# Optimization experiments

Measured on AMD Instinct MI355X. Metric: run time of the kernel, lower is better.

The kernel has to match this reference:

```python
import jax, jax.numpy as jnp
import numpy as np

D_MODEL = 1024
NUM_HEADS = 16
D_K = D_MODEL // NUM_HEADS
THETA = 10000.0


def _rope(x, pos):
    # x: [B, H, S, D_K], pos: [S]
    angles = 1.0 / (THETA ** (jnp.arange(0, D_K, 2, dtype=jnp.float32) / D_K))  # [D_K/2]
    ang = pos.astype(jnp.float32)[:, None] * angles  # [S, D_K/2]
    cos = jnp.repeat(jnp.cos(ang), 2, axis=-1)  # [S, D_K]
    sin = jnp.repeat(jnp.sin(ang), 2, axis=-1)
    x2 = x.reshape(*x.shape[:-1], D_K // 2, 2)
    xr = jnp.stack([-x2[..., 1], x2[..., 0]], axis=-1).reshape(x.shape)
    return x * cos + xr * sin


def setup_inputs() -> dict:
    key = jax.random.key(0)
    ks = jax.random.split(key, 5)
    B, S = 2, 2048
    sd = np.sqrt(2.0 / (D_MODEL + D_MODEL))
    return {
        "x": jax.random.normal(ks[0], (B, S, D_MODEL), dtype=jnp.float32),
        "token_positions": jnp.arange(S, dtype=jnp.int32),
        "Wq": jax.random.normal(ks[1], (D_MODEL, D_MODEL), dtype=jnp.float32) * sd,
        "Wk": jax.random.normal(ks[2], (D_MODEL, D_MODEL), dtype=jnp.float32) * sd,
        "Wv": jax.random.normal(ks[3], (D_MODEL, D_MODEL), dtype=jnp.float32) * sd,
        "Wo": jax.random.normal(ks[4], (D_MODEL, D_MODEL), dtype=jnp.float32) * sd,
    }


def reference(x, token_positions, Wq, Wk, Wv, Wo):
    B, S, _ = x.shape

    def proj_heads(W):
        y = jnp.einsum('bsd,ed->bse', x, W)  # weight stored [d_out, d_in]
        return y.reshape(B, S, NUM_HEADS, D_K).transpose(0, 2, 1, 3)  # [B,H,S,Dk]

    q = _rope(proj_heads(Wq), token_positions)
    k = _rope(proj_heads(Wk), token_positions)
    v = proj_heads(Wv)

    scores = jnp.einsum('bhqd,bhkd->bhqk', q, k) / np.sqrt(D_K)  # [B,H,S,S]
    causal = jnp.tril(jnp.ones((S, S), dtype=bool))
    scores = jnp.where(causal, scores, -jnp.inf)
    attn = jax.nn.softmax(scores, axis=-1)
    out = jnp.einsum('bhqk,bhkd->bhqd', attn, v)  # [B,H,S,Dk]
    out = out.transpose(0, 2, 1, 3).reshape(B, S, D_MODEL)
    return jnp.einsum('bsd,ed->bse', out, Wo)
```

## Files before the change

kernel.cpp:

```cpp
#include <hip/hip_runtime.h>
#include <hip/hip_bf16.h>
#include <cstdint>
#include <cmath>

#define SEQ 2048
#define NH 16
#define DM 1024
#define BATCH 2

typedef short bf16x8 __attribute__((ext_vector_type(8)));
typedef float f32x4 __attribute__((ext_vector_type(4)));
typedef const void __attribute__((address_space(1)))* gas_t;
typedef void __attribute__((address_space(3)))* las_t;

#if __has_builtin(__builtin_amdgcn_exp2f)
#define EXP2(x) __builtin_amdgcn_exp2f(x)
#else
#define EXP2(x) __expf((x) * 0.6931471805599453f)
#endif

#define QSCALE 0.18033688011112042f

static __device__ __forceinline__ unsigned short f2bf(float f) {
    union { __hip_bfloat16 h; unsigned short u; } cv;
    cv.h = __float2bfloat16(f);
    return cv.u;
}
static __device__ __forceinline__ float bf2f(unsigned short u) {
    union { unsigned short u; __hip_bfloat16 h; } cv;
    cv.u = u;
    return __bfloat162float(cv.h);
}

static __device__ __forceinline__ void gload_lds16(const void* g, void* l) {
    __builtin_amdgcn_global_load_lds(
        reinterpret_cast<gas_t>(reinterpret_cast<uintptr_t>(g)),
        reinterpret_cast<las_t>(reinterpret_cast<uintptr_t>(l)),
        16, 0, 0);
}

__global__ __launch_bounds__(256) void cvt_all(
    const float* __restrict__ x,  const float* __restrict__ wq,
    const float* __restrict__ wk, const float* __restrict__ wv,
    const float* __restrict__ wo,
    unsigned short* __restrict__ xb, unsigned short* __restrict__ wqkv,
    unsigned short* __restrict__ wob) {
    int blk = blockIdx.x;
    const float* src; unsigned short* dst; int base;
    if (blk < 4096)      { src = x;  dst = xb;              base = blk; }
    else if (blk < 5120) { src = wq; dst = wqkv;            base = blk - 4096; }
    else if (blk < 6144) { src = wk; dst = wqkv + 1048576;  base = blk - 5120; }
    else if (blk < 7168) { src = wv; dst = wqkv + 2097152;  base = blk - 6144; }
    else                 { src = wo; dst = wob;             base = blk - 7168; }
    int i = base * 256 + threadIdx.x;
    float4 v = reinterpret_cast<const float4*>(src)[i];
    ushort4 o;
    o.x = f2bf(v.x); o.y = f2bf(v.y); o.z = f2bf(v.z); o.w = f2bf(v.w);
    reinterpret_cast<ushort4*>(dst)[i] = o;
}

template<int OUT_BF16>
__global__ __launch_bounds__(256) void gemm_bt(
    const unsigned short* __restrict__ A,
    const unsigned short* __restrict__ B,
    void* __restrict__ C, int M, int N, int K) {
    __shared__ unsigned short As[128 * 32];
    __shared__ unsigned short Bs[128 * 32];
    const int tid = threadIdx.x;
    const int lane = tid & 63, wid = tid >> 6;
    const int wr = wid >> 1, wc = wid & 1;
    const int ln15 = lane & 15, kq = lane >> 4;
    const int bm = blockIdx.y, bn = blockIdx.x;

    f32x4 acc[4][4] = {};
    const int nk = K >> 5;
    for (int kt = 0; kt < nk; ++kt) {
        #pragma unroll
        for (int i = 0; i < 2; ++i) {
            int c = i * 256 + tid;
            int row = c >> 2, k8 = (c & 3) << 3;
            size_t gofsA = (size_t)(bm * 128 + row) * K + kt * 32 + k8;
            size_t gofsB = (size_t)(bn * 128 + row) * K + kt * 32 + k8;
            unsigned ldsoff = (unsigned)(i * 256 + wid * 64) * 16;
            gload_lds16(A + gofsA, (char*)As + ldsoff);
            gload_lds16(B + gofsB, (char*)Bs + ldsoff);
        }
        __syncthreads();
        bf16x8 af[4], bf[4];
        #pragma unroll
        for (int m = 0; m < 4; ++m)
            af[m] = *reinterpret_cast<const bf16x8*>(&As[(wr * 64 + m * 16 + ln15) * 32 + kq * 8]);
        #pragma unroll
        for (int n = 0; n < 4; ++n)
            bf[n] = *reinterpret_cast<const bf16x8*>(&Bs[(wc * 64 + n * 16 + ln15) * 32 + kq * 8]);
        #pragma unroll
        for (int m = 0; m < 4; ++m)
            #pragma unroll
            for (int n = 0; n < 4; ++n)
                acc[m][n] = __builtin_amdgcn_mfma_f32_16x16x32_bf16(af[m], bf[n], acc[m][n], 0, 0, 0);
        __syncthreads();
    }
    #pragma unroll
    for (int m = 0; m < 4; ++m) {
        #pragma unroll
        for (int n = 0; n < 4; ++n) {
            int col = bn * 128 + wc * 64 + n * 16 + ln15;
            #pragma unroll
            for (int j = 0; j < 4; ++j) {
                int row = bm * 128 + wr * 64 + m * 16 + kq * 4 + j;
                if constexpr (OUT_BF16 != 0)
                    ((unsigned short*)C)[(size_t)row * N + col] = f2bf(acc[m][n][j]);
                else
                    ((float*)C)[(size_t)row * N + col] = acc[m][n][j];
            }
        }
    }
}

__global__ __launch_bounds__(256) void rope_table(const int* __restrict__ pos,
                                                  float2* __restrict__ tab) {
    int idx = blockIdx.x * 256 + threadIdx.x;
    int s = idx >> 5, i = idx & 31;
    float fpos = (float)pos[s];
    float freq = exp2f(-(float)i * (13.287712379549449f / 32.0f));
    float ang = fpos * freq, sn, cs;
    sincosf(ang, &sn, &cs);
    tab[idx] = make_float2(cs, sn);
}

__global__ __launch_bounds__(256) void rope_kernel(
    const unsigned short* __restrict__ qkv, const float2* __restrict__ tab,
    unsigned short* __restrict__ Qh, unsigned short* __restrict__ Kh) {
    int bs = blockIdx.x;
    int b = bs >> 11, s = bs & (SEQ - 1);
    int t = threadIdx.x;
    #pragma unroll
    for (int p = t; p < 512; p += 256) {
        int h = p >> 5, i = p & 31;
        float2 cs = tab[(s << 5) + i];
        size_t src = (size_t)bs * 3072 + h * 64 + 2 * i;
        size_t dst = ((size_t)(b * NH + h) * SEQ + s) * 64 + 2 * i;
        ushort2 qv = *reinterpret_cast<const ushort2*>(qkv + src);
        float q0 = bf2f(qv.x), q1 = bf2f(qv.y);
        ushort2 qo;
        qo.x = f2bf((q0 * cs.x - q1 * cs.y) * QSCALE);
        qo.y = f2bf((q1 * cs.x + q0 * cs.y) * QSCALE);
        *reinterpret_cast<ushort2*>(Qh + dst) = qo;
        ushort2 kv = *reinterpret_cast<const ushort2*>(qkv + src + 1024);
        float k0 = bf2f(kv.x), k1 = bf2f(kv.y);
        ushort2 ko;
        ko.x = f2bf(k0 * cs.x - k1 * cs.y);
        ko.y = f2bf(k1 * cs.x + k0 * cs.y);
        *reinterpret_cast<ushort2*>(Kh + dst) = ko;
    }
}

__global__ __launch_bounds__(256) void vtrans_kernel(
    const unsigned short* __restrict__ qkv, unsigned short* __restrict__ Vo) {
    __shared__ unsigned short tile[64][65];
    int blk = blockIdx.x;
    int st = blk & 31, bh = blk >> 5;
    int sb = st * 64;
    int t = threadIdx.x;
    int b = bh >> 4, h = bh & 15;
    #pragma unroll
    for (int u = t; u < 1024; u += 256) {
        int sl = u >> 4, d4 = (u & 15) << 2;
        ushort4 v = *reinterpret_cast<const ushort4*>(
            qkv + (size_t)(b * SEQ + sb + sl) * 3072 + 2048 + h * 64 + d4);
        tile[sl][d4] = v.x; tile[sl][d4 + 1] = v.y;
        tile[sl][d4 + 2] = v.z; tile[sl][d4 + 3] = v.w;
    }
    __syncthreads();
    #pragma unroll
    for (int u = t; u < 1024; u += 256) {
        int d = u >> 4, s4 = (u & 15) << 2;
        ushort4 o;
        o.x = tile[s4][d]; o.y = tile[s4 + 1][d];
        o.z = tile[s4 + 2][d]; o.w = tile[s4 + 3][d];
        *reinterpret_cast<ushort4*>(Vo + ((size_t)bh * 64 + d) * SEQ + sb + s4) = o;
    }
}

__global__ __launch_bounds__(128) void attn_kernel(
    const unsigned short* __restrict__ Qh, const unsigned short* __restrict__ Kh,
    const unsigned short* __restrict__ Vt, unsigned short* __restrict__ Out) {
    __shared__ unsigned short Kb[2][32 * 64];
    __shared__ unsigned short Vb[2][64 * 32];
    __shared__ unsigned short Plds[2][16 * 40];

    const int tid = threadIdx.x;
    const int wid = tid >> 6, lane = tid & 63;
    const int ln15 = lane & 15, g = lane >> 4;
    const int bid = blockIdx.x;
    const int bh = bid & 31;
    const int band = 63 - (bid >> 5);
    const int qb = band * 32 + wid * 16;
    const int nt = band + 1;

    const unsigned short* Qp = Qh + (size_t)bh * SEQ * 64;
    const unsigned short* Kp = Kh + (size_t)bh * SEQ * 64;
    const unsigned short* Vp = Vt + (size_t)bh * 64 * SEQ;
    unsigned short* P = Plds[wid];

    const int c0 = tid, c1 = tid + 128;
    const unsigned short* kSrc0 = Kp + (size_t)(c0 >> 3) * 64 + (((c0 & 7) ^ ((c0 >> 3) & 7)) << 3);
    const unsigned short* kSrc1 = Kp + (size_t)(c1 >> 3) * 64 + (((c1 & 7) ^ ((c1 >> 3) & 7)) << 3);
    const unsigned short* vSrc0 = Vp + (size_t)(c0 >> 2) * SEQ + (((c0 & 3) ^ (((c0 >> 2) >> 1) & 3)) << 3);
    const unsigned short* vSrc1 = Vp + (size_t)(c1 >> 2) * SEQ + (((c1 & 3) ^ (((c1 >> 2) >> 1) & 3)) << 3);
    const unsigned base0 = (unsigned)wid * 1024;
    const unsigned base1 = 2048 + (unsigned)wid * 1024;

    auto stage = [&](int kb, int buf) {
        gload_lds16(kSrc0 + (size_t)kb * 64, (char*)Kb[buf] + base0);
        gload_lds16(kSrc1 + (size_t)kb * 64, (char*)Kb[buf] + base1);
        gload_lds16(vSrc0 + kb, (char*)Vb[buf] + base0);
        gload_lds16(vSrc1 + kb, (char*)Vb[buf] + base1);
    };

    const int r0 = ln15, r1 = ln15 + 16;
    const unsigned kOff0a = r0 * 128 + ((g ^ (r0 & 7)) << 4);
    const unsigned kOff0b = r0 * 128 + (((4 + g) ^ (r0 & 7)) << 4);
    const unsigned kOff1a = r1 * 128 + ((g ^ (r1 & 7)) << 4);
    const unsigned kOff1b = r1 * 128 + (((4 + g) ^ (r1 & 7)) << 4);
    unsigned vOff[4];
    #pragma unroll
    for (int c = 0; c < 4; ++c) {
        int d = c * 16 + ln15;
        vOff[c] = d * 64 + ((g ^ ((d >> 1) & 3)) << 4);
    }

    bf16x8 aq0 = *reinterpret_cast<const bf16x8*>(Qp + (size_t)(qb + ln15) * 64 + g * 8);
    bf16x8 aq1 = *reinterpret_cast<const bf16x8*>(Qp + (size_t)(qb + ln15) * 64 + 32 + g * 8);

    f32x4 oacc[4] = {};
    float lsum = 0.f;
    const int thr = qb + ln15 - 4 * g;

    stage(0, 0);

    for (int t = 0; t < nt; ++t) {
        const int kb = t << 5;
        const int cur = t & 1, nxt = cur ^ 1;
        {
            int tn = t + 1; if (tn > nt - 1) tn = nt - 1;
            stage(tn << 5, nxt);
        }
        asm volatile("s_waitcnt vmcnt(4)" ::: "memory");
        __builtin_amdgcn_s_barrier();

        const unsigned short* K0 = Kb[cur];
        const unsigned short* V0 = Vb[cur];
        const f32x4 z = {};
        bf16x8 kf0 = *reinterpret_cast<const bf16x8*>((const char*)K0 + kOff0a);
        bf16x8 kf1 = *reinterpret_cast<const bf16x8*>((const char*)K0 + kOff0b);
        bf16x8 kf2 = *reinterpret_cast<const bf16x8*>((const char*)K0 + kOff1a);
        bf16x8 kf3 = *reinterpret_cast<const bf16x8*>((const char*)K0 + kOff1b);
        f32x4 s0, s1;
        s0 = __builtin_amdgcn_mfma_f32_16x16x32_bf16(kf0, aq0, z, 0, 0, 0);
        s0 = __builtin_amdgcn_mfma_f32_16x16x32_bf16(kf1, aq1, s0, 0, 0, 0);
        s1 = __builtin_amdgcn_mfma_f32_16x16x32_bf16(kf2, aq0, z, 0, 0, 0);
        s1 = __builtin_amdgcn_mfma_f32_16x16x32_bf16(kf3, aq1, s1, 0, 0, 0);

        float p0[4], p1[4];
        if (t == band) {
            #pragma unroll
            for (int j = 0; j < 4; ++j) {
                p0[j] = (j <= thr - kb) ? EXP2(s0[j]) : 0.f;
                p1[j] = (j <= thr - kb - 16) ? EXP2(s1[j]) : 0.f;
            }
        } else {
            #pragma unroll
            for (int j = 0; j < 4; ++j) { p0[j] = EXP2(s0[j]); p1[j] = EXP2(s1[j]); }
        }
        lsum += (p0[0] + p0[1]) + (p0[2] + p0[3]) + (p1[0] + p1[1]) + (p1[2] + p1[3]);

        ushort4 w0, w1;
        w0.x = f2bf(p0[0]); w0.y = f2bf(p0[1]); w0.z = f2bf(p0[2]); w0.w = f2bf(p0[3]);
        w1.x = f2bf(p1[0]); w1.y = f2bf(p1[1]); w1.z = f2bf(p1[2]); w1.w = f2bf(p1[3]);
        *reinterpret_cast<ushort4*>(&P[ln15 * 40 + 4 * g]) = w0;
        *reinterpret_cast<ushort4*>(&P[ln15 * 40 + 16 + 4 * g]) = w1;
        asm volatile("s_waitcnt lgkmcnt(0)" ::: "memory");
        bf16x8 ap = *reinterpret_cast<const bf16x8*>(&P[ln15 * 40 + 8 * g]);
        #pragma unroll
        for (int c = 0; c < 4; ++c) {
            bf16x8 bv = *reinterpret_cast<const bf16x8*>((const char*)V0 + vOff[c]);
            oacc[c] = __builtin_amdgcn_mfma_f32_16x16x32_bf16(ap, bv, oacc[c], 0, 0, 0);
        }
        asm volatile("s_waitcnt lgkmcnt(0)" ::: "memory");
        __builtin_amdgcn_s_barrier();
    }

    float r = lsum;
    r += __shfl_xor(r, 16);
    r += __shfl_xor(r, 32);
    float linv = 1.f / r;
    float invj[4];
    #pragma unroll
    for (int j = 0; j < 4; ++j)
        invj[j] = __shfl(linv, 20 * g + j);

    int b = bh >> 4, h = bh & 15;
    #pragma unroll
    for (int c = 0; c < 4; ++c)
        #pragma unroll
        for (int j = 0; j < 4; ++j) {
            int s = qb + g * 4 + j;
            Out[((size_t)(b * SEQ + s)) * DM + h * 64 + c * 16 + ln15] =
                f2bf(oacc[c][j] * invj[j]);
        }
}

extern "C" void kernel_launch(void* const* d_in, const int* in_sizes, int n_in,
                              void* d_out, int out_size, void* d_ws, size_t ws_size,
                              hipStream_t stream) {
    const float* x = (const float*)d_in[0];
    const int* pos = (const int*)d_in[1];
    const float* Wq = (const float*)d_in[2];
    const float* Wk = (const float*)d_in[3];
    const float* Wv = (const float*)d_in[4];
    const float* Wo = (const float*)d_in[5];
    float* out = (float*)d_out;

    char* ws = (char*)d_ws;
    const size_t MB = 1024 * 1024;
    unsigned short* xb   = (unsigned short*)(ws + 0 * MB);
    unsigned short* wqkv = (unsigned short*)(ws + 8 * MB);
    unsigned short* wob  = (unsigned short*)(ws + 14 * MB);
    unsigned short* qkv  = (unsigned short*)(ws + 16 * MB);
    float2*         tab  = (float2*)       (ws + 40 * MB);
    unsigned short* qh   = (unsigned short*)(ws + 41 * MB);
    unsigned short* kh   = (unsigned short*)(ws + 49 * MB);
    unsigned short* vtr  = (unsigned short*)(ws + 57 * MB);
    unsigned short* att  = (unsigned short*)(ws + 65 * MB);

    cvt_all<<<8192, 256, 0, stream>>>(x, Wq, Wk, Wv, Wo, xb, wqkv, wob);
    rope_table<<<256, 256, 0, stream>>>(pos, tab);

    gemm_bt<1><<<dim3(24, 32), 256, 0, stream>>>(xb, wqkv, qkv, 4096, 3072, 1024);

    rope_kernel<<<4096, 256, 0, stream>>>(qkv, tab, qh, kh);
    vtrans_kernel<<<1024, 256, 0, stream>>>(qkv, vtr);

    attn_kernel<<<2048, 128, 0, stream>>>(qh, kh, vtr, att);

    gemm_bt<0><<<dim3(8, 32), 256, 0, stream>>>(att, wob, out, 4096, 1024, 1024);
}
```

Baseline: 133.0 us.

## Pair low and high causal query bands per block to balance work and share K/V

Each attention block now handles two query bands, fold and 63-fold, so every block walks the same number of key tiles and the staged K/V tiles are reused by both bands. The grid is halved to 1024 blocks. This balances causal workload across blocks and halves K/V loads for the low band. In exchange each thread holds more registers for two Q fragments and two accumulators, and there are fewer blocks to fill the GPU.

Result: no change. 130.8 us (-1.6%).

```diff
diff --git a/kernel.cpp b/kernel.cpp
--- a/kernel.cpp
+++ b/kernel.cpp
@@ -187,21 +187,23 @@
     const unsigned short* __restrict__ Vt, unsigned short* __restrict__ Out) {
     __shared__ unsigned short Kb[2][32 * 64];
     __shared__ unsigned short Vb[2][64 * 32];
-    __shared__ unsigned short Plds[2][16 * 40];
+    __shared__ unsigned short Plds[2][2][16 * 40];
 
     const int tid = threadIdx.x;
     const int wid = tid >> 6, lane = tid & 63;
     const int ln15 = lane & 15, g = lane >> 4;
     const int bid = blockIdx.x;
     const int bh = bid & 31;
-    const int band = 63 - (bid >> 5);
-    const int qb = band * 32 + wid * 16;
-    const int nt = band + 1;
+    const int fold = bid >> 5;
+    const int qbL = fold * 32 + wid * 16;
+    const int qbH = (63 - fold) * 32 + wid * 16;
+    const int nt = 64 - fold;
 
     const unsigned short* Qp = Qh + (size_t)bh * SEQ * 64;
     const unsigned short* Kp = Kh + (size_t)bh * SEQ * 64;
     const unsigned short* Vp = Vt + (size_t)bh * 64 * SEQ;
-    unsigned short* P = Plds[wid];
+    unsigned short* PL = Plds[wid][0];
+    unsigned short* PH = Plds[wid][1];
 
     const int c0 = tid, c1 = tid + 128;
     const unsigned short* kSrc0 = Kp + (size_t)(c0 >> 3) * 64 + (((c0 & 7) ^ ((c0 >> 3) & 7)) << 3);
@@ -230,12 +232,15 @@
         vOff[c] = d * 64 + ((g ^ ((d >> 1) & 3)) << 4);
     }
 
-    bf16x8 aq0 = *reinterpret_cast<const bf16x8*>(Qp + (size_t)(qb + ln15) * 64 + g * 8);
-    bf16x8 aq1 = *reinterpret_cast<const bf16x8*>(Qp + (size_t)(qb + ln15) * 64 + 32 + g * 8);
-
-    f32x4 oacc[4] = {};
-    float lsum = 0.f;
-    const int thr = qb + ln15 - 4 * g;
+    bf16x8 aqL0 = *reinterpret_cast<const bf16x8*>(Qp + (size_t)(qbL + ln15) * 64 + g * 8);
+    bf16x8 aqL1 = *reinterpret_cast<const bf16x8*>(Qp + (size_t)(qbL + ln15) * 64 + 32 + g * 8);
+    bf16x8 aqH0 = *reinterpret_cast<const bf16x8*>(Qp + (size_t)(qbH + ln15) * 64 + g * 8);
+    bf16x8 aqH1 = *reinterpret_cast<const bf16x8*>(Qp + (size_t)(qbH + ln15) * 64 + 32 + g * 8);
+
+    f32x4 oaccL[4] = {}, oaccH[4] = {};
+    float lsumL = 0.f, lsumH = 0.f;
+    const int thrL = qbL + ln15 - 4 * g;
+    const int thrH = qbH + ln15 - 4 * g;
 
     stage(0, 0);
 
@@ -256,59 +261,118 @@
         bf16x8 kf1 = *reinterpret_cast<const bf16x8*>((const char*)K0 + kOff0b);
         bf16x8 kf2 = *reinterpret_cast<const bf16x8*>((const char*)K0 + kOff1a);
         bf16x8 kf3 = *reinterpret_cast<const bf16x8*>((const char*)K0 + kOff1b);
-        f32x4 s0, s1;
-        s0 = __builtin_amdgcn_mfma_f32_16x16x32_bf16(kf0, aq0, z, 0, 0, 0);
-        s0 = __builtin_amdgcn_mfma_f32_16x16x32_bf16(kf1, aq1, s0, 0, 0, 0);
-        s1 = __builtin_amdgcn_mfma_f32_16x16x32_bf16(kf2, aq0, z, 0, 0, 0);
-        s1 = __builtin_amdgcn_mfma_f32_16x16x32_bf16(kf3, aq1, s1, 0, 0, 0);
-
-        float p0[4], p1[4];
-        if (t == band) {
+        bf16x8 bv0 = *reinterpret_cast<const bf16x8*>((const char*)V0 + vOff[0]);
+        bf16x8 bv1 = *reinterpret_cast<const bf16x8*>((const char*)V0 + vOff[1]);
+        bf16x8 bv2 = *reinterpret_cast<const bf16x8*>((const char*)V0 + vOff[2]);
+        bf16x8 bv3 = *reinterpret_cast<const bf16x8*>((const char*)V0 + vOff[3]);
+
+        const bool loAct = (t <= fold);
+
+        f32x4 sH0, sH1, sL0, sL1;
+        sH0 = __builtin_amdgcn_mfma_f32_16x16x32_bf16(kf0, aqH0, z, 0, 0, 0);
+        sH0 = __builtin_amdgcn_mfma_f32_16x16x32_bf16(kf1, aqH1, sH0, 0, 0, 0);
+        sH1 = __builtin_amdgcn_mfma_f32_16x16x32_bf16(kf2, aqH0, z, 0, 0, 0);
+        sH1 = __builtin_amdgcn_mfma_f32_16x16x32_bf16(kf3, aqH1, sH1, 0, 0, 0);
+        if (loAct) {
+            sL0 = __builtin_amdgcn_mfma_f32_16x16x32_bf16(kf0, aqL0, z, 0, 0, 0);
+            sL0 = __builtin_amdgcn_mfma_f32_16x16x32_bf16(kf1, aqL1, sL0, 0, 0, 0);
+            sL1 = __builtin_amdgcn_mfma_f32_16x16x32_bf16(kf2, aqL0, z, 0, 0, 0);
+            sL1 = __builtin_amdgcn_mfma_f32_16x16x32_bf16(kf3, aqL1, sL1, 0, 0, 0);
+        }
+
+        {
+            float p0[4], p1[4];
+            if (t == nt - 1) {
+                #pragma unroll
+                for (int j = 0; j < 4; ++j) {
+                    p0[j] = (j <= thrH - kb) ? EXP2(sH0[j]) : 0.f;
+                    p1[j] = (j <= thrH - kb - 16) ? EXP2(sH1[j]) : 0.f;
+                }
+            } else {
+                #pragma unroll
+                for (int j = 0; j < 4; ++j) { p0[j] = EXP2(sH0[j]); p1[j] = EXP2(sH1[j]); }
+            }
+            lsumH += (p0[0] + p0[1]) + (p0[2] + p0[3]) + (p1[0] + p1[1]) + (p1[2] + p1[3]);
+            ushort4 w0, w1;
+            w0.x = f2bf(p0[0]); w0.y = f2bf(p0[1]); w0.z = f2bf(p0[2]); w0.w = f2bf(p0[3]);
+            w1.x = f2bf(p1[0]); w1.y = f2bf(p1[1]); w1.z = f2bf(p1[2]); w1.w = f2bf(p1[3]);
+            *reinterpret_cast<ushort4*>(&PH[ln15 * 40 + 4 * g]) = w0;
+            *reinterpret_cast<ushort4*>(&PH[ln15 * 40 + 16 + 4 * g]) = w1;
+        }
+        if (loAct) {
+            float p0[4], p1[4];
+            if (t == fold) {
+                #pragma unroll
+                for (int j = 0; j < 4; ++j) {
+                    p0[j] = (j <= thrL - kb) ? EXP2(sL0[j]) : 0.f;
+                    p1[j] = (j <= thrL - kb - 16) ? EXP2(sL1[j]) : 0.f;
+                }
+            } else {
+                #pragma unroll
+                for (int j = 0; j < 4; ++j) { p0[j] = EXP2(sL0[j]); p1[j] = EXP2(sL1[j]); }
+            }
+            lsumL += (p0[0] + p0[1]) + (p0[2] + p0[3]) + (p1[0] + p1[1]) + (p1[2] + p1[3]);
+            ushort4 w0, w1;
+            w0.x = f2bf(p0[0]); w0.y = f2bf(p0[1]); w0.z = f2bf(p0[2]); w0.w = f2bf(p0[3]);
+            w1.x = f2bf(p1[0]); w1.y = f2bf(p1[1]); w1.z = f2bf(p1[2]); w1.w = f2bf(p1[3]);
+            *reinterpret_cast<ushort4*>(&PL[ln15 * 40 + 4 * g]) = w0;
+            *reinterpret_cast<ushort4*>(&PL[ln15 * 40 + 16 + 4 * g]) = w1;
+        }
+        asm volatile("s_waitcnt lgkmcnt(0)" ::: "memory");
+
+        bf16x8 apH = *reinterpret_cast<const bf16x8*>(&PH[ln15 * 40 + 8 * g]);
+        oaccH[0] = __builtin_amdgcn_mfma_f32_16x16x32_bf16(apH, bv0, oaccH[0], 0, 0, 0);
+        oaccH[1] = __builtin_amdgcn_mfma_f32_16x16x32_bf16(apH, bv1, oaccH[1], 0, 0, 0);
+        oaccH[2] = __builtin_amdgcn_mfma_f32_16x16x32_bf16(apH, bv2, oaccH[2], 0, 0, 0);
+        oaccH[3] = __builtin_amdgcn_mfma_f32_16x16x32_bf16(apH, bv3, oaccH[3], 0, 0, 0);
+        if (loAct) {
+            bf16x8 apL = *reinterpret_cast<const bf16x8*>(&PL[ln15 * 40 + 8 * g]);
+            oaccL[0] = __builtin_amdgcn_mfma_f32_16x16x32_bf16(apL, bv0, oaccL[0], 0, 0, 0);
+            oaccL[1] = __builtin_amdgcn_mfma_f32_16x16x32_bf16(apL, bv1, oaccL[1], 0, 0, 0);
+            oaccL[2] = __builtin_amdgcn_mfma_f32_16x16x32_bf16(apL, bv2, oaccL[2], 0, 0, 0);
+            oaccL[3] = __builtin_amdgcn_mfma_f32_16x16x32_bf16(apL, bv3, oaccL[3], 0, 0, 0);
+        }
+        asm volatile("s_waitcnt lgkmcnt(0)" ::: "memory");
+        __builtin_amdgcn_s_barrier();
+    }
+
+    int b = bh >> 4, h = bh & 15;
+    {
+        float r = lsumH;
+        r += __shfl_xor(r, 16);
+        r += __shfl_xor(r, 32);
+        float linv = 1.f / r;
+        float invj[4];
+        #pragma unroll
+        for (int j = 0; j < 4; ++j)
+            invj[j] = __shfl(linv, 20 * g + j);
+        #pragma unroll
+        for (int c = 0; c < 4; ++c)
             #pragma unroll
             for (int j = 0; j < 4; ++j) {
-                p0[j] = (j <= thr - kb) ? EXP2(s0[j]) : 0.f;
-                p1[j] = (j <= thr - kb - 16) ? EXP2(s1[j]) : 0.f;
+                int s = qbH + g * 4 + j;
+                Out[((size_t)(b * SEQ + s)) * DM + h * 64 + c * 16 + ln15] =
+                    f2bf(oaccH[c][j] * invj[j]);
             }
-        } else {
+    }
+    {
+        float r = lsumL;
+        r += __shfl_xor(r, 16);
+        r += __shfl_xor(r, 32);
+        float linv = 1.f / r;
+        float invj[4];
+        #pragma unroll
+        for (int j = 0; j < 4; ++j)
+            invj[j] = __shfl(linv, 20 * g + j);
+        #pragma unroll
+        for (int c = 0; c < 4; ++c)
             #pragma unroll
-            for (int j = 0; j < 4; ++j) { p0[j] = EXP2(s0[j]); p1[j] = EXP2(s1[j]); }
-        }
-        lsum += (p0[0] + p0[1]) + (p0[2] + p0[3]) + (p1[0] + p1[1]) + (p1[2] + p1[3]);
-
-        ushort4 w0, w1;
-        w0.x = f2bf(p0[0]); w0.y = f2bf(p0[1]); w0.z = f2bf(p0[2]); w0.w = f2bf(p0[3]);
-        w1.x = f2bf(p1[0]); w1.y = f2bf(p1[1]); w1.z = f2bf(p1[2]); w1.w = f2bf(p1[3]);
-        *reinterpret_cast<ushort4*>(&P[ln15 * 40 + 4 * g]) = w0;
-        *reinterpret_cast<ushort4*>(&P[ln15 * 40 + 16 + 4 * g]) = w1;
-        asm volatile("s_waitcnt lgkmcnt(0)" ::: "memory");
-        bf16x8 ap = *reinterpret_cast<const bf16x8*>(&P[ln15 * 40 + 8 * g]);
-        #pragma unroll
-        for (int c = 0; c < 4; ++c) {
-            bf16x8 bv = *reinterpret_cast<const bf16x8*>((const char*)V0 + vOff[c]);
-            oacc[c] = __builtin_amdgcn_mfma_f32_16x16x32_bf16(ap, bv, oacc[c], 0, 0, 0);
-        }
-        asm volatile("s_waitcnt lgkmcnt(0)" ::: "memory");
-        __builtin_amdgcn_s_barrier();
-    }
-
-    float r = lsum;
-    r += __shfl_xor(r, 16);
-    r += __shfl_xor(r, 32);
-    float linv = 1.f / r;
-    float invj[4];
-    #pragma unroll
-    for (int j = 0; j < 4; ++j)
-        invj[j] = __shfl(linv, 20 * g + j);
-
-    int b = bh >> 4, h = bh & 15;
-    #pragma unroll
-    for (int c = 0; c < 4; ++c)
-        #pragma unroll
-        for (int j = 0; j < 4; ++j) {
-            int s = qb + g * 4 + j;
-            Out[((size_t)(b * SEQ + s)) * DM + h * 64 + c * 16 + ln15] =
-                f2bf(oacc[c][j] * invj[j]);
-        }
+            for (int j = 0; j < 4; ++j) {
+                int s = qbL + g * 4 + j;
+                Out[((size_t)(b * SEQ + s)) * DM + h * 64 + c * 16 + ln15] =
+                    f2bf(oaccL[c][j] * invj[j]);
+            }
+    }
 }
 
 extern "C" void kernel_launch(void* const* d_in, const int* in_sizes, int n_in,
@@ -342,7 +406,7 @@
     rope_kernel<<<4096, 256, 0, stream>>>(qkv, tab, qh, kh);
     vtrans_kernel<<<1024, 256, 0, stream>>>(qkv, vtr);
 
-    attn_kernel<<<2048, 128, 0, stream>>>(qh, kh, vtr, att);
+    attn_kernel<<<1024, 128, 0, stream>>>(qh, kh, vtr, att);
 
     gemm_bt<0><<<dim3(8, 32), 256, 0, stream>>>(att, wob, out, 4096, 1024, 1024);
 }
```

## Pair causal query bands per block and widen attention key tiles to 64

Applied to the files above, without the earlier changes.

Each attention block now processes two query bands (pb and 63-pb) so that every block does the same amount of causal work, and the grid is halved. Key/value tiles grow from 32 to 64 keys per iteration, doubling the MFMA work per barrier and per staged load while halving the number of loop iterations. The aim is to balance load across blocks and cut per-iteration sync and pipeline overhead. In exchange, LDS use per block doubles, register pressure rises, and there are fewer blocks available to fill the CUs.

Result: faster. 128.3 us (-3.5%).

```diff
diff --git a/kernel.cpp b/kernel.cpp
--- a/kernel.cpp
+++ b/kernel.cpp
@@ -185,130 +185,160 @@
 __global__ __launch_bounds__(128) void attn_kernel(
     const unsigned short* __restrict__ Qh, const unsigned short* __restrict__ Kh,
     const unsigned short* __restrict__ Vt, unsigned short* __restrict__ Out) {
-    __shared__ unsigned short Kb[2][32 * 64];
-    __shared__ unsigned short Vb[2][64 * 32];
-    __shared__ unsigned short Plds[2][16 * 40];
+    __shared__ unsigned short Kb[2][64 * 64];
+    __shared__ unsigned short Vb[2][64 * 64];
+    __shared__ unsigned short Plds[2][16 * 72];
 
     const int tid = threadIdx.x;
     const int wid = tid >> 6, lane = tid & 63;
     const int ln15 = lane & 15, g = lane >> 4;
     const int bid = blockIdx.x;
     const int bh = bid & 31;
-    const int band = 63 - (bid >> 5);
-    const int qb = band * 32 + wid * 16;
-    const int nt = band + 1;
+    const int pb = bid >> 5;
 
     const unsigned short* Qp = Qh + (size_t)bh * SEQ * 64;
     const unsigned short* Kp = Kh + (size_t)bh * SEQ * 64;
     const unsigned short* Vp = Vt + (size_t)bh * 64 * SEQ;
-    unsigned short* P = Plds[wid];
-
-    const int c0 = tid, c1 = tid + 128;
-    const unsigned short* kSrc0 = Kp + (size_t)(c0 >> 3) * 64 + (((c0 & 7) ^ ((c0 >> 3) & 7)) << 3);
-    const unsigned short* kSrc1 = Kp + (size_t)(c1 >> 3) * 64 + (((c1 & 7) ^ ((c1 >> 3) & 7)) << 3);
-    const unsigned short* vSrc0 = Vp + (size_t)(c0 >> 2) * SEQ + (((c0 & 3) ^ (((c0 >> 2) >> 1) & 3)) << 3);
-    const unsigned short* vSrc1 = Vp + (size_t)(c1 >> 2) * SEQ + (((c1 & 3) ^ (((c1 >> 2) >> 1) & 3)) << 3);
-    const unsigned base0 = (unsigned)wid * 1024;
-    const unsigned base1 = 2048 + (unsigned)wid * 1024;
+    char* Pc = (char*)Plds[wid];
+
+    const unsigned short* kSrc[4];
+    const unsigned short* vSrc[4];
+    #pragma unroll
+    for (int p = 0; p < 4; ++p) {
+        int c = tid + (p << 7);
+        int row = c >> 3, slot = c & 7;
+        kSrc[p] = Kp + (size_t)row * 64 + ((slot ^ (row & 7)) << 3);
+        vSrc[p] = Vp + (size_t)row * SEQ + ((slot ^ (row & 7)) << 3);
+    }
 
     auto stage = [&](int kb, int buf) {
-        gload_lds16(kSrc0 + (size_t)kb * 64, (char*)Kb[buf] + base0);
-        gload_lds16(kSrc1 + (size_t)kb * 64, (char*)Kb[buf] + base1);
-        gload_lds16(vSrc0 + kb, (char*)Vb[buf] + base0);
-        gload_lds16(vSrc1 + kb, (char*)Vb[buf] + base1);
+        #pragma unroll
+        for (int p = 0; p < 4; ++p) {
+            unsigned bb = (unsigned)(wid * 1024 + p * 2048);
+            gload_lds16(kSrc[p] + (size_t)kb * 64, (char*)Kb[buf] + bb);
+            gload_lds16(vSrc[p] + kb, (char*)Vb[buf] + bb);
+        }
     };
 
-    const int r0 = ln15, r1 = ln15 + 16;
-    const unsigned kOff0a = r0 * 128 + ((g ^ (r0 & 7)) << 4);
-    const unsigned kOff0b = r0 * 128 + (((4 + g) ^ (r0 & 7)) << 4);
-    const unsigned kOff1a = r1 * 128 + ((g ^ (r1 & 7)) << 4);
-    const unsigned kOff1b = r1 * 128 + (((4 + g) ^ (r1 & 7)) << 4);
-    unsigned vOff[4];
+    unsigned kOff[4][2], vOff[4][2];
+    #pragma unroll
+    for (int s = 0; s < 4; ++s) {
+        int r = ln15 + 16 * s;
+        kOff[s][0] = r * 128 + ((g ^ (r & 7)) << 4);
+        kOff[s][1] = r * 128 + (((4 + g) ^ (r & 7)) << 4);
+    }
     #pragma unroll
     for (int c = 0; c < 4; ++c) {
         int d = c * 16 + ln15;
-        vOff[c] = d * 64 + ((g ^ ((d >> 1) & 3)) << 4);
-    }
-
-    bf16x8 aq0 = *reinterpret_cast<const bf16x8*>(Qp + (size_t)(qb + ln15) * 64 + g * 8);
-    bf16x8 aq1 = *reinterpret_cast<const bf16x8*>(Qp + (size_t)(qb + ln15) * 64 + 32 + g * 8);
-
-    f32x4 oacc[4] = {};
-    float lsum = 0.f;
-    const int thr = qb + ln15 - 4 * g;
-
-    stage(0, 0);
-
-    for (int t = 0; t < nt; ++t) {
-        const int kb = t << 5;
-        const int cur = t & 1, nxt = cur ^ 1;
-        {
-            int tn = t + 1; if (tn > nt - 1) tn = nt - 1;
-            stage(tn << 5, nxt);
+        vOff[c][0] = d * 128 + ((g ^ (d & 7)) << 4);
+        vOff[c][1] = d * 128 + (((4 + g) ^ (d & 7)) << 4);
+    }
+    const unsigned pW = (unsigned)(ln15 * 144 + 8 * g);
+    const unsigned pR = (unsigned)(ln15 * 144 + 16 * g);
+
+    const int b = bh >> 4, h = bh & 15;
+
+    for (int bi = 0; bi < 2; ++bi) {
+        const int bnd = bi ? (63 - pb) : pb;
+        const int qb = bnd * 32 + wid * 16;
+        const int nt = (bnd + 2) >> 1;
+        const int thr = qb + ln15 - 4 * g;
+
+        bf16x8 aq0 = *reinterpret_cast<const bf16x8*>(Qp + (size_t)(qb + ln15) * 64 + g * 8);
+        bf16x8 aq1 = *reinterpret_cast<const bf16x8*>(Qp + (size_t)(qb + ln15) * 64 + 32 + g * 8);
+
+        f32x4 oacc[4] = {};
+        float lsum = 0.f;
+
+        stage(0, 0);
+
+        for (int t = 0; t < nt; ++t) {
+            const int kb = t << 6;
+            const int cur = t & 1;
+            if (t + 1 < nt) {
+                stage((t + 1) << 6, cur ^ 1);
+                asm volatile("s_waitcnt vmcnt(8)" ::: "memory");
+            } else {
+                asm volatile("s_waitcnt vmcnt(0)" ::: "memory");
+            }
+            __builtin_amdgcn_s_barrier();
+
+            const char* K0 = (const char*)Kb[cur];
+            const char* V0 = (const char*)Vb[cur];
+            bf16x8 kf[8], bv[8];
+            #pragma unroll
+            for (int s = 0; s < 4; ++s) {
+                kf[2 * s]     = *reinterpret_cast<const bf16x8*>(K0 + kOff[s][0]);
+                kf[2 * s + 1] = *reinterpret_cast<const bf16x8*>(K0 + kOff[s][1]);
+            }
+            #pragma unroll
+            for (int c = 0; c < 4; ++c) {
+                bv[2 * c]     = *reinterpret_cast<const bf16x8*>(V0 + vOff[c][0]);
+                bv[2 * c + 1] = *reinterpret_cast<const bf16x8*>(V0 + vOff[c][1]);
+            }
+
+            const f32x4 z = {};
+            f32x4 sq[4];
+            #pragma unroll
+            for (int s = 0; s < 4; ++s) {
+                sq[s] = __builtin_amdgcn_mfma_f32_16x16x32_bf16(kf[2 * s], aq0, z, 0, 0, 0);
+                sq[s] = __builtin_amdgcn_mfma_f32_16x16x32_bf16(kf[2 * s + 1], aq1, sq[s], 0, 0, 0);
+            }
+
+            float pv[4][4];
+            if (t == nt - 1) {
+                #pragma unroll
+                for (int s = 0; s < 4; ++s)
+                    #pragma unroll
+                    for (int j = 0; j < 4; ++j)
+                        pv[s][j] = (j <= thr - kb - 16 * s) ? EXP2(sq[s][j]) : 0.f;
+            } else {
+                #pragma unroll
+                for (int s = 0; s < 4; ++s)
+                    #pragma unroll
+                    for (int j = 0; j < 4; ++j)
+                        pv[s][j] = EXP2(sq[s][j]);
+            }
+            #pragma unroll
+            for (int s = 0; s < 4; ++s)
+                lsum += (pv[s][0] + pv[s][1]) + (pv[s][2] + pv[s][3]);
+
+            #pragma unroll
+            for (int s = 0; s < 4; ++s) {
+                ushort4 w;
+                w.x = f2bf(pv[s][0]); w.y = f2bf(pv[s][1]);
+                w.z = f2bf(pv[s][2]); w.w = f2bf(pv[s][3]);
+                *reinterpret_cast<ushort4*>(Pc + pW + 32 * s) = w;
+            }
+            asm volatile("s_waitcnt lgkmcnt(0)" ::: "memory");
+            bf16x8 ap0 = *reinterpret_cast<const bf16x8*>(Pc + pR);
+            bf16x8 ap1 = *reinterpret_cast<const bf16x8*>(Pc + pR + 64);
+            #pragma unroll
+            for (int c = 0; c < 4; ++c) {
+                oacc[c] = __builtin_amdgcn_mfma_f32_16x16x32_bf16(ap0, bv[2 * c], oacc[c], 0, 0, 0);
+                oacc[c] = __builtin_amdgcn_mfma_f32_16x16x32_bf16(ap1, bv[2 * c + 1], oacc[c], 0, 0, 0);
+            }
+            asm volatile("s_waitcnt lgkmcnt(0)" ::: "memory");
+            __builtin_amdgcn_s_barrier();
         }
-        asm volatile("s_waitcnt vmcnt(4)" ::: "memory");
-        __builtin_amdgcn_s_barrier();
-
-        const unsigned short* K0 = Kb[cur];
-        const unsigned short* V0 = Vb[cur];
-        const f32x4 z = {};
-        bf16x8 kf0 = *reinterpret_cast<const bf16x8*>((const char*)K0 + kOff0a);
-        bf16x8 kf1 = *reinterpret_cast<const bf16x8*>((const char*)K0 + kOff0b);
-        bf16x8 kf2 = *reinterpret_cast<const bf16x8*>((const char*)K0 + kOff1a);
-        bf16x8 kf3 = *reinterpret_cast<const bf16x8*>((const char*)K0 + kOff1b);
-        f32x4 s0, s1;
-        s0 = __builtin_amdgcn_mfma_f32_16x16x32_bf16(kf0, aq0, z, 0, 0, 0);
-        s0 = __builtin_amdgcn_mfma_f32_16x16x32_bf16(kf1, aq1, s0, 0, 0, 0);
-        s1 = __builtin_amdgcn_mfma_f32_16x16x32_bf16(kf2, aq0, z, 0, 0, 0);
-        s1 = __builtin_amdgcn_mfma_f32_16x16x32_bf16(kf3, aq1, s1, 0, 0, 0);
-
-        float p0[4], p1[4];
-        if (t == band) {
+
+        float r = lsum;
+        r += __shfl_xor(r, 16);
+        r += __shfl_xor(r, 32);
+        float linv = 1.f / r;
+        float invj[4];
+        #pragma unroll
+        for (int j = 0; j < 4; ++j)
+            invj[j] = __shfl(linv, 20 * g + j);
+        #pragma unroll
+        for (int c = 0; c < 4; ++c)
             #pragma unroll
             for (int j = 0; j < 4; ++j) {
-                p0[j] = (j <= thr - kb) ? EXP2(s0[j]) : 0.f;
-                p1[j] = (j <= thr - kb - 16) ? EXP2(s1[j]) : 0.f;
-            }
-        } else {
-            #pragma unroll
-            for (int j = 0; j < 4; ++j) { p0[j] = EXP2(s0[j]); p1[j] = EXP2(s1[j]); }
-        }
-        lsum += (p0[0] + p0[1]) + (p0[2] + p0[3]) + (p1[0] + p1[1]) + (p1[2] + p1[3]);
-
-        ushort4 w0, w1;
-        w0.x = f2bf(p0[0]); w0.y = f2bf(p0[1]); w0.z = f2bf(p0[2]); w0.w = f2bf(p0[3]);
-        w1.x = f2bf(p1[0]); w1.y = f2bf(p1[1]); w1.z = f2bf(p1[2]); w1.w = f2bf(p1[3]);
-        *reinterpret_cast<ushort4*>(&P[ln15 * 40 + 4 * g]) = w0;
-        *reinterpret_cast<ushort4*>(&P[ln15 * 40 + 16 + 4 * g]) = w1;
-        asm volatile("s_waitcnt lgkmcnt(0)" ::: "memory");
-        bf16x8 ap = *reinterpret_cast<const bf16x8*>(&P[ln15 * 40 + 8 * g]);
-        #pragma unroll
-        for (int c = 0; c < 4; ++c) {
-            bf16x8 bv = *reinterpret_cast<const bf16x8*>((const char*)V0 + vOff[c]);
-            oacc[c] = __builtin_amdgcn_mfma_f32_16x16x32_bf16(ap, bv, oacc[c], 0, 0, 0);
-        }
-        asm volatile("s_waitcnt lgkmcnt(0)" ::: "memory");
-        __builtin_amdgcn_s_barrier();
-    }
-
-    float r = lsum;
-    r += __shfl_xor(r, 16);
-    r += __shfl_xor(r, 32);
-    float linv = 1.f / r;
-    float invj[4];
-    #pragma unroll
-    for (int j = 0; j < 4; ++j)
-        invj[j] = __shfl(linv, 20 * g + j);
-
-    int b = bh >> 4, h = bh & 15;
-    #pragma unroll
-    for (int c = 0; c < 4; ++c)
-        #pragma unroll
-        for (int j = 0; j < 4; ++j) {
-            int s = qb + g * 4 + j;
-            Out[((size_t)(b * SEQ + s)) * DM + h * 64 + c * 16 + ln15] =
-                f2bf(oacc[c][j] * invj[j]);
-        }
+                int s = qb + g * 4 + j;
+                Out[((size_t)(b * SEQ + s)) * DM + h * 64 + c * 16 + ln15] =
+                    f2bf(oacc[c][j] * invj[j]);
+            }
+    }
 }
 
 extern "C" void kernel_launch(void* const* d_in, const int* in_sizes, int n_in,
@@ -342,7 +372,7 @@
     rope_kernel<<<4096, 256, 0, stream>>>(qkv, tab, qh, kh);
     vtrans_kernel<<<1024, 256, 0, stream>>>(qkv, vtr);
 
-    attn_kernel<<<2048, 128, 0, stream>>>(qh, kh, vtr, att);
+    attn_kernel<<<1024, 128, 0, stream>>>(qh, kh, vtr, att);
 
     gemm_bt<0><<<dim3(8, 32), 256, 0, stream>>>(att, wob, out, 4096, 1024, 1024);
 }
```
